# Kernel optimization log

Hardware: AMD Instinct MI355X
Metric: run time of the kernel (lower is better)

The kernel has to match this reference:

```python
import jax, jax.numpy as jnp
import numpy as np

NEG = -9.0e15


def setup_inputs() -> dict:
    key = jax.random.key(0)
    k_x, k_w, k_e, k_b, k_m = jax.random.split(key, 5)
    B, N, C, F = 2048, 64, 256, 256
    x = jax.random.normal(k_x, (B, N, C), dtype=jnp.float32)
    W = jax.random.normal(k_w, (2, C, F), dtype=jnp.float32) * (1.414 / np.sqrt(C + F))
    # full logit tensor; only entries where mask holds are ever read (equivalent
    # to torch's flat `e` scattered into the nonzero positions of adj)
    e = jax.random.normal(k_e, (F, N, N), dtype=jnp.float32)
    bias = jax.random.normal(k_b, (F,), dtype=jnp.float32) * (1.0 / np.sqrt(C))
    # symmetric adjacency mask with self-loops, density ~0.3
    m = jax.random.bernoulli(k_m, 0.3, (N, N))
    mask = (m | m.T) | jnp.eye(N, dtype=bool)
    return {"x": x, "W": W, "e": e, "bias": bias, "mask": mask}


def reference(x, W, e, bias, mask):
    # x: [B,N,C], W: [2,C,F], e: [F,N,N], bias: [F], mask: [N,N] bool
    h0 = x @ W[0]                                   # [B,N,F] (self term)
    h1 = x @ W[1]                                   # [B,N,F] (neighbor term)
    logits = jnp.where(mask[None, :, :], e, NEG)    # [F,N,N]
    adj = jax.nn.softmax(logits, axis=2)            # per-channel row softmax
    N = mask.shape[0]
    eye = jnp.eye(N, dtype=bool)
    d = jnp.diagonal(adj, axis1=1, axis2=2)         # [F,N]  (adj * E diagonal)
    off = jnp.where(eye[None, :, :], 0.0, adj)      # [F,N,N] (adj * (1-E))
    # (adj*E) @ h0 reduces to per-node diagonal scaling; off-diag is a
    # per-channel NxN matmul batched over B.
    out = d.T[None, :, :] * h0 + jnp.einsum('fnm,bmf->bnf', off, h1)
    return out + bias[None, None, :]
```

## Files before the change

kernel.cpp:

```cpp
#include <hip/hip_runtime.h>
#include <hip/hip_bf16.h>


typedef __attribute__((ext_vector_type(8))) short  fragA;
typedef __attribute__((ext_vector_type(4))) float  f32x4;
typedef __attribute__((ext_vector_type(8))) unsigned short u16x8;
typedef __attribute__((ext_vector_type(4))) unsigned short u16x4;

constexpr long OFF_OFF = 0;
constexpr long OFF_WT  = 2l * 1024 * 1024;
constexpr long OFF_DS  = OFF_WT + 512l * 256 * 2;
constexpr long OFF_XB  = OFF_DS + 64l * 256 * 4;
constexpr long WS_NEED = OFF_XB + 131072l * 256 * 2;

static __device__ inline unsigned short f2bf(float f) {
  __hip_bfloat16 h = __float2bfloat16(f);
  return __builtin_bit_cast(unsigned short, h);
}
static __device__ inline float bf2f(unsigned short u) {
  unsigned int x = ((unsigned int)u) << 16;
  return __builtin_bit_cast(float, x);
}

__global__ __launch_bounds__(256) void k_pre(const float* __restrict__ x,
                                             const float* __restrict__ e,
                                             const float* __restrict__ W,
                                             const unsigned char* __restrict__ mask,
                                             char* __restrict__ ws_b) {
  const int bid = blockIdx.x;
  const int tid = threadIdx.x;
  if (bid < 4096) {
    unsigned short* off = (unsigned short*)(ws_b + OFF_OFF);
    float* dscale = (float*)(ws_b + OFF_DS);
    const int lane = tid & 63;
    const int row  = bid * 4 + (tid >> 6);
    const int n = row & 63;
    bool is_u8 = __all(mask[lane * 65] != 0);
    bool mv;
    if (is_u8) mv = mask[n * 64 + lane] != 0;
    else       mv = ((const int*)mask)[n * 64 + lane] != 0;
    float v = mv ? e[(long)row * 64 + lane] : -1e30f;
    float mx = v;
#pragma unroll
    for (int s = 32; s; s >>= 1) mx = fmaxf(mx, __shfl_xor(mx, s));
    float ex = mv ? __expf(v - mx) : 0.f;
    float sm = ex;
#pragma unroll
    for (int s = 32; s; s >>= 1) sm += __shfl_xor(sm, s);
    float adj = ex / sm;
    const int f = row >> 6;
    if (lane == n) dscale[n * 256 + f] = adj;
    off[(long)row * 64 + lane] = f2bf(lane == n ? 0.f : adj);
  } else if (bid < 6144) {
    unsigned short* xb = (unsigned short*)(ws_b + OFF_XB);
    long i = ((long)(bid - 4096) * 256 + tid) * 8;
    const long stride = 2048l * 256 * 8;
    const long total = 131072l * 256;
    for (; i < total; i += stride) {
      float4 a = *(const float4*)(x + i);
      float4 b = *(const float4*)(x + i + 4);
      u16x8 p;
      p[0] = f2bf(a.x); p[1] = f2bf(a.y); p[2] = f2bf(a.z); p[3] = f2bf(a.w);
      p[4] = f2bf(b.x); p[5] = f2bf(b.y); p[6] = f2bf(b.z); p[7] = f2bf(b.w);
      *(u16x8*)(xb + i) = p;
    }
  } else {
    unsigned short* Wt = (unsigned short*)(ws_b + OFF_WT);
    __shared__ float t[64][65];
    const int b2 = bid - 6144;
    const int w = b2 >> 4, f0 = ((b2 >> 2) & 3) * 64, c0 = (b2 & 3) * 64;
    const int tr = tid >> 2, tc = (tid & 3) * 16;
    const float* src = W + ((long)(w * 256 + c0 + tr)) * 256 + f0 + tc;
#pragma unroll
    for (int i = 0; i < 16; i += 4) {
      float4 v = *(const float4*)(src + i);
      t[tr][tc + i] = v.x; t[tr][tc + i + 1] = v.y;
      t[tr][tc + i + 2] = v.z; t[tr][tc + i + 3] = v.w;
    }
    __syncthreads();
    u16x8 p0, p1;
#pragma unroll
    for (int i = 0; i < 8; i++)  p0[i] = f2bf(t[tc + i][tr]);
#pragma unroll
    for (int i = 0; i < 8; i++)  p1[i] = f2bf(t[tc + 8 + i][tr]);
    unsigned short* dst = Wt + ((long)(w * 256 + f0 + tr)) * 256 + c0 + tc;
    *(u16x8*)dst = p0;
    *(u16x8*)(dst + 8) = p1;
  }
}

__global__ __launch_bounds__(256, 3) void k_main(const float* __restrict__ bias,
                                                 const char* __restrict__ ws_b,
                                                 float* __restrict__ out) {
  const unsigned short* Wt   = (const unsigned short*)(ws_b + OFF_WT);
  const unsigned short* offp = (const unsigned short*)(ws_b + OFF_OFF);
  const unsigned short* xb   = (const unsigned short*)(ws_b + OFF_XB);
  const float* dscale        = (const float*)(ws_b + OFF_DS);

  __shared__ __align__(16) unsigned short Bs[64 * 264];
  __shared__ __align__(16) unsigned short Hb[32 * 296];

  const int tid = threadIdx.x;
  const int wid = tid >> 6, lane = tid & 63;
  const int lr = lane & 15, qu = lane >> 4;

  const int wg = blockIdx.x;
  const int xcd = wg & 7, s = wg >> 3;
  const int bb = xcd * 64 + (s >> 3);
  const int fb = s & 7;
  const int f0 = fb * 32;
  const long R0 = (long)bb * 256;
  const long Rw = R0 + wid * 64;

  {
    int col = tid & 63, kc = (tid >> 6) * 64;
    int wrow = (col < 32) ? (f0 + col) : (256 + f0 + col - 32);
    const unsigned short* src = Wt + (long)wrow * 256 + kc;
    unsigned short* d = &Bs[col * 264 + kc];
#pragma unroll
    for (int i = 0; i < 8; i++)
      *(u16x8*)(d + i * 8) = *(const u16x8*)(src + i * 8);
  }
  __syncthreads();

  f32x4 acc[4][4] = {};
  const unsigned short* ax = xb + (Rw + lr) * 256 + qu * 8;
  fragA a_cur[4], a_nxt[4];
#pragma unroll
  for (int i = 0; i < 4; i++) a_cur[i] = *(const fragA*)(ax + i * 4096);
#pragma unroll
  for (int ks = 0; ks < 8; ks++) {
    if (ks < 7) {
#pragma unroll
      for (int i = 0; i < 4; i++)
        a_nxt[i] = *(const fragA*)(ax + i * 4096 + (ks + 1) * 32);
    }
    fragA bfr[4];
#pragma unroll
    for (int j = 0; j < 4; j++)
      bfr[j] = *(const fragA*)&Bs[(j * 16 + lr) * 264 + ks * 32 + qu * 8];
#pragma unroll
    for (int i = 0; i < 4; i++)
#pragma unroll
      for (int j = 0; j < 4; j++)
        acc[i][j] = __builtin_amdgcn_mfma_f32_16x16x32_bf16(a_cur[i], bfr[j], acc[i][j], 0, 0, 0);
#pragma unroll
    for (int i = 0; i < 4; i++) a_cur[i] = a_nxt[i];
  }

#pragma unroll
  for (int i = 0; i < 4; i++) {
#pragma unroll
    for (int j = 2; j < 4; j++) {
      int fl = (j - 2) * 16 + lr;
      int m  = i * 16 + qu * 4;
      u16x4 pk;
      pk[0] = f2bf(acc[i][j][0]); pk[1] = f2bf(acc[i][j][1]);
      pk[2] = f2bf(acc[i][j][2]); pk[3] = f2bf(acc[i][j][3]);
      *(u16x4*)&Hb[fl * 296 + wid * 72 + m] = pk;
    }
  }
  __syncthreads();

  for (int q = 0; q < 8; q++) {
    int fl = wid * 8 + q;
    long fg = f0 + fl;
    const unsigned short* ob = offp + fg * 4096;
    fragA a0 = *(const fragA*)&Hb[fl * 296 + (lr & 3) * 72 + qu * 8];
    fragA a1 = *(const fragA*)&Hb[fl * 296 + (lr & 3) * 72 + 32 + qu * 8];
    fragA b0[4], b1[4];
#pragma unroll
    for (int ct = 0; ct < 4; ct++) {
      b0[ct] = *(const fragA*)(ob + (ct * 16 + lr) * 64 + qu * 8);
      b1[ct] = *(const fragA*)(ob + (ct * 16 + lr) * 64 + 32 + qu * 8);
    }
    f32x4 ea[4] = {};
#pragma unroll
    for (int ct = 0; ct < 4; ct++) {
      ea[ct] = __builtin_amdgcn_mfma_f32_16x16x32_bf16(a0, b0[ct], ea[ct], 0, 0, 0);
      ea[ct] = __builtin_amdgcn_mfma_f32_16x16x32_bf16(a1, b1[ct], ea[ct], 0, 0, 0);
    }
    if (qu == 0) {
#pragma unroll
      for (int ct = 0; ct < 4; ct++)
#pragma unroll
        for (int r = 0; r < 4; r++)
          Hb[fl * 296 + r * 72 + ct * 16 + lr] = f2bf(ea[ct][r]);
    }
  }
  __syncthreads();

#pragma unroll
  for (int i = 0; i < 4; i++) {
#pragma unroll
    for (int j = 0; j < 2; j++) {
      int c = j * 16 + lr;
      int f = f0 + c;
      float bs = bias[f];
#pragma unroll
      for (int r = 0; r < 4; r++) {
        int m = i * 16 + qu * 4 + r;
        float ev = bf2f(Hb[c * 296 + wid * 72 + m]);
        out[(Rw + m) * 256 + f] = dscale[m * 256 + f] * acc[i][j][r] + ev + bs;
      }
    }
  }
}

extern "C" void kernel_launch(void* const* d_in, const int* in_sizes, int n_in,
                              void* d_out, int out_size, void* d_ws, size_t ws_size,
                              hipStream_t stream) {
  const float* x    = (const float*)d_in[0];
  const float* W    = (const float*)d_in[1];
  const float* e    = (const float*)d_in[2];
  const float* bias = (const float*)d_in[3];
  const unsigned char* mask = (const unsigned char*)d_in[4];
  float* out = (float*)d_out;
  char* ws = (char*)d_ws;
  if (ws_size < (size_t)WS_NEED) return;

  k_pre<<<6176, 256, 0, stream>>>(x, e, W, mask, ws);
  k_main<<<4096, 256, 0, stream>>>(bias, ws, out);
}
```

Baseline: 239.7 us.

## Halve row tile, stage x and W via async global-to-LDS loads with swizzle

The main kernel now processes 128 rows (two batch elements) per workgroup instead of 256 and launches twice as many workgroups. The x tile and the W slice are staged into LDS with global_load_lds direct copies using an XOR swizzle, and the K loop is split into four LDS-resident chunks instead of streaming A fragments from global memory in registers. The neighbor aggregation swaps the MFMA operand roles so the off-diagonal matrix is the A operand, which changes how results are written back. This cuts per-thread register use and aims for better occupancy and coalesced loads, at the cost of more W reloads per output and extra barriers in the K loop.

```diff
diff --git a/kernel.cpp b/kernel.cpp
--- a/kernel.cpp
+++ b/kernel.cpp
@@ -20,6 +20,14 @@
 static __device__ inline float bf2f(unsigned short u) {
   unsigned int x = ((unsigned int)u) << 16;
   return __builtin_bit_cast(float, x);
+}
+static __device__ __forceinline__ void gl16(const void* g, void* l) {
+  __builtin_amdgcn_global_load_lds(
+      (const __attribute__((address_space(1))) unsigned int*)g,
+      (__attribute__((address_space(3))) unsigned int*)l, 16, 0, 0);
+}
+static __device__ __forceinline__ f32x4 mfma16(fragA a, fragA b, f32x4 c) {
+  return __builtin_amdgcn_mfma_f32_16x16x32_bf16(a, b, c, 0, 0, 0);
 }
 
 __global__ __launch_bounds__(256) void k_pre(const float* __restrict__ x,
@@ -89,119 +97,134 @@
   }
 }
 
-__global__ __launch_bounds__(256, 3) void k_main(const float* __restrict__ bias,
-                                                 const char* __restrict__ ws_b,
-                                                 float* __restrict__ out) {
-  const unsigned short* Wt   = (const unsigned short*)(ws_b + OFF_WT);
+__global__ __launch_bounds__(256) void k_main(const float* __restrict__ bias,
+                                              const char* __restrict__ ws_b,
+                                              float* __restrict__ out) {
   const unsigned short* offp = (const unsigned short*)(ws_b + OFF_OFF);
-  const unsigned short* xb   = (const unsigned short*)(ws_b + OFF_XB);
   const float* dscale        = (const float*)(ws_b + OFF_DS);
-
-  __shared__ __align__(16) unsigned short Bs[64 * 264];
-  __shared__ __align__(16) unsigned short Hb[32 * 296];
+  const char* xb_b = ws_b + OFF_XB;
+  const char* wt_b = ws_b + OFF_WT;
+
+  __shared__ __align__(16) char arena[49152];
+  unsigned short* Hb = (unsigned short*)arena;
 
   const int tid = threadIdx.x;
   const int wid = tid >> 6, lane = tid & 63;
   const int lr = lane & 15, qu = lane >> 4;
 
   const int wg = blockIdx.x;
-  const int xcd = wg & 7, s = wg >> 3;
-  const int bb = xcd * 64 + (s >> 3);
-  const int fb = s & 7;
-  const int f0 = fb * 32;
-  const long R0 = (long)bb * 256;
-  const long Rw = R0 + wid * 64;
+  const int f0 = (wg & 7) * 32;
+  const long R0 = (long)(wg >> 3) * 128;
 
   {
-    int col = tid & 63, kc = (tid >> 6) * 64;
-    int wrow = (col < 32) ? (f0 + col) : (256 + f0 + col - 32);
-    const unsigned short* src = Wt + (long)wrow * 256 + kc;
-    unsigned short* d = &Bs[col * 264 + kc];
-#pragma unroll
-    for (int i = 0; i < 8; i++)
-      *(u16x8*)(d + i * 8) = *(const u16x8*)(src + i * 8);
+    const int c  = tid >> 5;
+    const int cb = (tid & 31) * 16;
+    const int sw = cb ^ ((c & 7) << 4);
+#pragma unroll
+    for (int i = 0; i < 8; i++) {
+      int col  = i * 8 + c;
+      int wrow = (col < 32) ? (f0 + col) : (224 + f0 + col);
+      gl16(wt_b + (long)wrow * 512 + sw, arena + 16384 + i * 4096 + tid * 16);
+    }
+  }
+  const int ar = tid >> 3;
+  const int aswz = ((tid & 7) ^ (ar & 7)) << 4;
+#pragma unroll
+  for (int i = 0; i < 4; i++)
+    gl16(xb_b + (R0 + i * 32 + ar) * 512 + aswz, arena + i * 4096 + tid * 16);
+
+  f32x4 acc[2][4] = {};
+  const int arow0 = wid * 32;
+
+  for (int ks = 0; ks < 4; ks++) {
+    __syncthreads();
+    fragA af[2][2], bf_[2][4];
+#pragma unroll
+    for (int kk = 0; kk < 2; kk++) {
+#pragma unroll
+      for (int i2 = 0; i2 < 2; i2++) {
+        int r = arow0 + i2 * 16 + lr;
+        af[kk][i2] = *(const fragA*)(arena + r * 128 +
+                        ((kk * 64 + qu * 16) ^ ((lr & 7) << 4)));
+      }
+#pragma unroll
+      for (int j = 0; j < 4; j++) {
+        int cc = j * 16 + lr;
+        bf_[kk][j] = *(const fragA*)(arena + 16384 + cc * 512 +
+                        ((ks * 128 + kk * 64 + qu * 16) ^ ((lr & 7) << 4)));
+      }
+    }
+#pragma unroll
+    for (int kk = 0; kk < 2; kk++)
+#pragma unroll
+      for (int i2 = 0; i2 < 2; i2++)
+#pragma unroll
+        for (int j = 0; j < 4; j++)
+          acc[i2][j] = mfma16(af[kk][i2], bf_[kk][j], acc[i2][j]);
+    __syncthreads();
+    if (ks < 3) {
+#pragma unroll
+      for (int i = 0; i < 4; i++)
+        gl16(xb_b + (R0 + i * 32 + ar) * 512 + (ks + 1) * 128 + aswz,
+             arena + i * 4096 + tid * 16);
+    }
+  }
+
+  const int hb_b = wid >> 1;
+  const int hm0 = (wid & 1) * 32;
+#pragma unroll
+  for (int j = 2; j < 4; j++) {
+#pragma unroll
+    for (int i2 = 0; i2 < 2; i2++) {
+      int f = (j - 2) * 16 + lr;
+      int m = hm0 + i2 * 16 + qu * 4;
+      u16x4 pk;
+      pk[0] = f2bf(acc[i2][j][0]); pk[1] = f2bf(acc[i2][j][1]);
+      pk[2] = f2bf(acc[i2][j][2]); pk[3] = f2bf(acc[i2][j][3]);
+      *(u16x4*)(Hb + f * 136 + hb_b * 64 + m) = pk;
+    }
   }
   __syncthreads();
 
-  f32x4 acc[4][4] = {};
-  const unsigned short* ax = xb + (Rw + lr) * 256 + qu * 8;
-  fragA a_cur[4], a_nxt[4];
-#pragma unroll
-  for (int i = 0; i < 4; i++) a_cur[i] = *(const fragA*)(ax + i * 4096);
-#pragma unroll
-  for (int ks = 0; ks < 8; ks++) {
-    if (ks < 7) {
-#pragma unroll
-      for (int i = 0; i < 4; i++)
-        a_nxt[i] = *(const fragA*)(ax + i * 4096 + (ks + 1) * 32);
-    }
-    fragA bfr[4];
-#pragma unroll
-    for (int j = 0; j < 4; j++)
-      bfr[j] = *(const fragA*)&Bs[(j * 16 + lr) * 264 + ks * 32 + qu * 8];
-#pragma unroll
-    for (int i = 0; i < 4; i++)
-#pragma unroll
-      for (int j = 0; j < 4; j++)
-        acc[i][j] = __builtin_amdgcn_mfma_f32_16x16x32_bf16(a_cur[i], bfr[j], acc[i][j], 0, 0, 0);
-#pragma unroll
-    for (int i = 0; i < 4; i++) a_cur[i] = a_nxt[i];
-  }
-
-#pragma unroll
-  for (int i = 0; i < 4; i++) {
-#pragma unroll
-    for (int j = 2; j < 4; j++) {
-      int fl = (j - 2) * 16 + lr;
-      int m  = i * 16 + qu * 4;
-      u16x4 pk;
-      pk[0] = f2bf(acc[i][j][0]); pk[1] = f2bf(acc[i][j][1]);
-      pk[2] = f2bf(acc[i][j][2]); pk[3] = f2bf(acc[i][j][3]);
-      *(u16x4*)&Hb[fl * 296 + wid * 72 + m] = pk;
-    }
-  }
-  __syncthreads();
-
+#pragma unroll 2
   for (int q = 0; q < 8; q++) {
     int fl = wid * 8 + q;
-    long fg = f0 + fl;
-    const unsigned short* ob = offp + fg * 4096;
-    fragA a0 = *(const fragA*)&Hb[fl * 296 + (lr & 3) * 72 + qu * 8];
-    fragA a1 = *(const fragA*)&Hb[fl * 296 + (lr & 3) * 72 + 32 + qu * 8];
-    fragA b0[4], b1[4];
-#pragma unroll
-    for (int ct = 0; ct < 4; ct++) {
-      b0[ct] = *(const fragA*)(ob + (ct * 16 + lr) * 64 + qu * 8);
-      b1[ct] = *(const fragA*)(ob + (ct * 16 + lr) * 64 + 32 + qu * 8);
-    }
+    const unsigned short* ob = offp + (long)(f0 + fl) * 4096;
     f32x4 ea[4] = {};
 #pragma unroll
-    for (int ct = 0; ct < 4; ct++) {
-      ea[ct] = __builtin_amdgcn_mfma_f32_16x16x32_bf16(a0, b0[ct], ea[ct], 0, 0, 0);
-      ea[ct] = __builtin_amdgcn_mfma_f32_16x16x32_bf16(a1, b1[ct], ea[ct], 0, 0, 0);
-    }
-    if (qu == 0) {
-#pragma unroll
-      for (int ct = 0; ct < 4; ct++)
-#pragma unroll
-        for (int r = 0; r < 4; r++)
-          Hb[fl * 296 + r * 72 + ct * 16 + lr] = f2bf(ea[ct][r]);
+    for (int kk = 0; kk < 2; kk++) {
+      fragA hbf = *(const fragA*)(Hb + fl * 136 + (lr & 1) * 64 + kk * 32 + qu * 8);
+#pragma unroll
+      for (int ct = 0; ct < 4; ct++) {
+        fragA of = *(const fragA*)(ob + (ct * 16 + lr) * 64 + kk * 32 + qu * 8);
+        ea[ct] = mfma16(of, hbf, ea[ct]);
+      }
+    }
+    if (lr < 2) {
+#pragma unroll
+      for (int ct = 0; ct < 4; ct++) {
+        u16x4 pk;
+        pk[0] = f2bf(ea[ct][0]); pk[1] = f2bf(ea[ct][1]);
+        pk[2] = f2bf(ea[ct][2]); pk[3] = f2bf(ea[ct][3]);
+        *(u16x4*)(Hb + fl * 136 + lr * 64 + ct * 16 + qu * 4) = pk;
+      }
     }
   }
   __syncthreads();
 
 #pragma unroll
-  for (int i = 0; i < 4; i++) {
-#pragma unroll
-    for (int j = 0; j < 2; j++) {
-      int c = j * 16 + lr;
-      int f = f0 + c;
-      float bs = bias[f];
+  for (int j = 0; j < 2; j++) {
+    int f = f0 + j * 16 + lr;
+    float bs = bias[f];
+#pragma unroll
+    for (int i2 = 0; i2 < 2; i2++) {
+      int n0 = hm0 + i2 * 16 + qu * 4;
+      u16x4 ev = *(const u16x4*)(Hb + (j * 16 + lr) * 136 + hb_b * 64 + n0);
 #pragma unroll
       for (int r = 0; r < 4; r++) {
-        int m = i * 16 + qu * 4 + r;
-        float ev = bf2f(Hb[c * 296 + wid * 72 + m]);
-        out[(Rw + m) * 256 + f] = dscale[m * 256 + f] * acc[i][j][r] + ev + bs;
+        int rowloc = arow0 + i2 * 16 + qu * 4 + r;
+        out[(R0 + rowloc) * 256 + f] =
+            dscale[(n0 + r) * 256 + f] * acc[i2][j][r] + bf2f(ev[r]) + bs;
       }
     }
   }
@@ -220,5 +243,5 @@
   if (ws_size < (size_t)WS_NEED) return;
 
   k_pre<<<6176, 256, 0, stream>>>(x, e, W, mask, ws);
-  k_main<<<4096, 256, 0, stream>>>(bias, ws, out);
-}
+  k_main<<<8192, 256, 0, stream>>>(bias, ws, out);
+}
```

Result: slower. 309.7 us (+29.2%).
